# Optimization experiments

Measured on AMD Instinct MI355X. Metric: run time of the kernel, lower is better.

Reference implementation:

```python
import jax, jax.numpy as jnp
import numpy as np

B, L, D = 2, 2048, 768
H = 12
HD = D // H  # 64
SCALE = HD ** -0.5


def setup_inputs() -> dict:
    key = jax.random.key(0)
    k1, k2, k3 = jax.random.split(key, 3)
    x = jax.random.normal(k1, (B, L, D), dtype=jnp.float32)
    mask = jnp.ones((B, L), dtype=jnp.int32)
    # nn.Linear weights: [out_features, in_features]
    Wqkv = jax.random.normal(k2, (3 * D, D), dtype=jnp.float32) * (D ** -0.5)
    bqkv = jnp.zeros((3 * D,), dtype=jnp.float32)
    Wout = jax.random.normal(k3, (D, D), dtype=jnp.float32) * (D ** -0.5)
    bout = jnp.zeros((D,), dtype=jnp.float32)
    return {"x": x, "mask": mask, "Wqkv": Wqkv, "bqkv": bqkv, "Wout": Wout, "bout": bout}


def reference(x, mask, Wqkv, bqkv, Wout, bout):
    Bx, Lx, Dx = x.shape
    # qkv projection: [B,L,3D] -> [3,B,H,L,HD]
    qkv = x @ Wqkv.T + bqkv
    qkv = qkv.reshape(Bx, Lx, 3, H, HD).transpose(2, 0, 3, 1, 4)
    q, k, v = qkv[0], qkv[1], qkv[2]
    # scores [B,H,L,L]
    attn = jnp.einsum('bhqd,bhkd->bhqk', q, k) * SCALE
    attn = jnp.where(mask[:, None, None, :] == 0, -jnp.inf, attn)
    attn = jax.nn.softmax(attn, axis=-1)
    # dropout p=0.0 -> identity
    out = jnp.einsum('bhqk,bhkd->bhqd', attn, v)
    out = out.transpose(0, 2, 1, 3).reshape(Bx, Lx, Dx)
    return out @ Wout.T + bout
```

## Files before the change

### kernel.cpp

```cpp
#include <hip/hip_runtime.h>
#include <hip/hip_bf16.h>

#define DEV __device__ __forceinline__

typedef __bf16 bf16_t;
typedef bf16_t bf16x8 __attribute__((ext_vector_type(8)));
typedef float f32x4 __attribute__((ext_vector_type(4)));
typedef float f32x16 __attribute__((ext_vector_type(16)));
typedef unsigned int u32x4 __attribute__((ext_vector_type(4)));

constexpr int Bc = 2, Lc = 2048, Dc = 768, Hc = 12, HDc = 64;
constexpr int NTOK = Bc * Lc;
constexpr int QKVN = 3 * Dc;
constexpr float ATT_SCALE = 0.125f;
constexpr float LOG2E = 1.44269504088896f;

DEV unsigned short f2bf(float f) {
  unsigned int u = __builtin_bit_cast(unsigned int, f);
  u += 0x7FFFu + ((u >> 16) & 1u);
  return (unsigned short)(u >> 16);
}

DEV bf16x8 ld16(const unsigned short* p) {
  return __builtin_bit_cast(bf16x8, *reinterpret_cast<const u32x4*>(p));
}

DEV unsigned cvtpk(float lo, float hi) {
  unsigned r;
  asm("v_cvt_pk_bf16_f32 %0, %1, %2" : "=v"(r) : "v"(lo), "v"(hi));
  return r;
}

DEV void gload16(const unsigned short* g, unsigned short* l) {
  __builtin_amdgcn_global_load_lds(
      (const __attribute__((address_space(1))) unsigned int*)g,
      (__attribute__((address_space(3))) unsigned int*)l, 16, 0, 0);
}

__global__ __launch_bounds__(256) void prep_kernel(
    const float* __restrict__ x, const float* __restrict__ Wqkv,
    const float* __restrict__ Wout, const int* __restrict__ mask,
    unsigned short* __restrict__ xb, unsigned short* __restrict__ wqkvb,
    unsigned short* __restrict__ woutb, float* __restrict__ mb,
    int* __restrict__ mflag) {
  const int bid = blockIdx.x, tid = threadIdx.x;
  const float* src; unsigned short* dst; int base;
  if (bid < 3072)      { src = x;    dst = xb;    base = bid; }
  else if (bid < 4800) { src = Wqkv; dst = wqkvb; base = bid - 3072; }
  else if (bid < 5376) { src = Wout; dst = woutb; base = bid - 4800; }
  else {
    int i = (bid - 5376) * 256 + tid;
    int mv = mask[i];
    mb[i] = mv ? 0.f : -1e30f;
    unsigned long long anyz = __ballot(mv == 0);
    if ((tid & 63) == 0) mflag[i >> 6] = (anyz != 0ull) ? 1 : 0;
    return;
  }
  int i = (base * 256 + tid) * 4;
  float4 v = *reinterpret_cast<const float4*>(src + i);
  ushort4 o;
  o.x = f2bf(v.x); o.y = f2bf(v.y); o.z = f2bf(v.z); o.w = f2bf(v.w);
  *reinterpret_cast<ushort4*>(dst + i) = o;
}

template <int MODE>
__global__ __launch_bounds__(256) void gemm_bt(
    const unsigned short* __restrict__ A,
    const unsigned short* __restrict__ Bw,
    const float* __restrict__ bias,
    unsigned short* __restrict__ qb, unsigned short* __restrict__ kb,
    unsigned short* __restrict__ vtb,
    float* __restrict__ Y,
    int M, int N, int K) {
  constexpr int BM = 128, BN = 128, BK = 64;
  __shared__ alignas(16) unsigned short a_lds[BM * BK];
  __shared__ alignas(16) unsigned short b_lds[BN * BK];
  __shared__ alignas(16) unsigned short qk_patch[(MODE == 0) ? 4 : 1][16][72];

  const int tid = threadIdx.x;
  const int lane = tid & 63;
  const int l15 = lane & 15, lg = lane >> 4;
  const int wave = tid >> 6;
  const int wr = wave >> 1, wc = wave & 1;

  const int ntiles = N / BN;
  const int m0 = (blockIdx.x / ntiles) * BM;
  const int n0 = (blockIdx.x % ntiles) * BN;

  f32x4 acc[4][4] = {};

  for (int k0 = 0; k0 < K; k0 += BK) {
#pragma unroll
    for (int i = 0; i < 4; ++i) {
      int cc = i * 256 + tid;
      int row = cc >> 3, col = (cc & 7) * 8;
      gload16(A + (size_t)(m0 + row) * K + k0 + col, &a_lds[(i * 256 + wave * 64) * 8]);
      gload16(Bw + (size_t)(n0 + row) * K + k0 + col, &b_lds[(i * 256 + wave * 64) * 8]);
    }
    __syncthreads();
#pragma unroll
    for (int kk = 0; kk < 2; ++kk) {
      bf16x8 af[4], bfr[4];
#pragma unroll
      for (int m = 0; m < 4; ++m) {
        int row = wr * 64 + m * 16 + l15;
        af[m] = ld16(&a_lds[row * BK + kk * 32 + lg * 8]);
      }
#pragma unroll
      for (int n = 0; n < 4; ++n) {
        int row = wc * 64 + n * 16 + l15;
        bfr[n] = ld16(&b_lds[row * BK + kk * 32 + lg * 8]);
      }
#pragma unroll
      for (int m = 0; m < 4; ++m)
#pragma unroll
        for (int n = 0; n < 4; ++n)
          acc[m][n] = __builtin_amdgcn_mfma_f32_16x16x32_bf16(af[m], bfr[n], acc[m][n], 0, 0, 0);
    }
    __syncthreads();
  }

  if constexpr (MODE == 0) {
    const int base_col = n0 + wc * 64;
    const int s = base_col / Dc;
    const int h = (base_col % Dc) >> 6;
    if (s == 2) {
#pragma unroll
      for (int m = 0; m < 4; ++m) {
        int lq = m0 + wr * 64 + m * 16 + lg * 4;
        int b = lq >> 11, lql = lq & 2047;
#pragma unroll
        for (int n = 0; n < 4; ++n) {
          int d = n * 16 + l15;
          float bv = bias[base_col + n * 16 + l15];
          ushort4 o;
#pragma unroll
          for (int j = 0; j < 4; ++j)
            ((unsigned short*)&o)[j] = f2bf(acc[m][n][j] + bv);
          *reinterpret_cast<ushort4*>(
              vtb + ((size_t)(b * Hc + h) * HDc + d) * Lc + lql) = o;
        }
      }
    } else {
      unsigned short* dst = (s == 0) ? qb : kb;
      const float sc = (s == 0) ? (ATT_SCALE * LOG2E) : 1.0f;
#pragma unroll
      for (int m = 0; m < 4; ++m) {
#pragma unroll
        for (int n = 0; n < 4; ++n) {
          float bv = bias[base_col + n * 16 + l15];
#pragma unroll
          for (int j = 0; j < 4; ++j)
            qk_patch[wave][lg * 4 + j][n * 16 + l15] =
                f2bf((acc[m][n][j] + bv) * sc);
        }
#pragma unroll
        for (int i = 0; i < 2; ++i) {
          int task = i * 64 + lane;
          int r = task >> 3, ch = task & 7;
          int lq = m0 + wr * 64 + m * 16 + r;
          int b = lq >> 11, lql = lq & 2047;
          u32x4 v = *reinterpret_cast<const u32x4*>(&qk_patch[wave][r][ch * 8]);
          *reinterpret_cast<u32x4*>(
              dst + ((size_t)(b * Hc + h) * Lc + lql) * HDc + ch * 8) = v;
        }
      }
    }
  } else {
#pragma unroll
    for (int m = 0; m < 4; ++m) {
      int row_base = m0 + wr * 64 + m * 16 + lg * 4;
#pragma unroll
      for (int n = 0; n < 4; ++n) {
        int col = n0 + wc * 64 + n * 16 + l15;
        float bv = bias[col];
#pragma unroll
        for (int j = 0; j < 4; ++j)
          Y[(size_t)(row_base + j) * Dc + col] = acc[m][n][j] + bv;
      }
    }
  }
}

__global__ __launch_bounds__(512) void attn_kernel(
    const unsigned short* __restrict__ qb,
    const unsigned short* __restrict__ kb,
    const unsigned short* __restrict__ vtb,
    const float* __restrict__ mb,
    const int* __restrict__ mflag,
    unsigned short* __restrict__ aout) {
  __shared__ alignas(16) unsigned short k_lds[2][2][4096];
  __shared__ alignas(16) unsigned short v_lds[2][2][4096];
  __shared__ float l_lds[4][32];
  const int tid = threadIdx.x;
  const int lane = tid & 63;
  const int l31 = lane & 31;
  const int hi = lane >> 5;
  const int wave = tid >> 6;
  const int g = wave >> 2;
  const int ws = wave & 3;
  const int f = blockIdx.x;
  const int loc = f >> 3;
  const int bh = (f & 7) * 3 + (loc >> 4);
  const int b = bh / Hc, h = bh % Hc;
  const int q0 = (loc & 15) * 128 + ws * 32;
  const int kvbase = g * (Lc / 2);

  const unsigned short* Kbh = kb + (size_t)bh * Lc * HDc;
  const unsigned short* Vbh = vtb + (size_t)bh * HDc * Lc;
  const float* mbb = mb + b * Lc + kvbase + hi * 4;
  const int* mfp = mflag + b * (Lc / 64) + (kvbase >> 6);

  bf16x8 qf[4];
  {
    const unsigned short* Qp = qb + ((size_t)bh * Lc + q0 + l31) * HDc + hi * 8;
#pragma unroll
    for (int c = 0; c < 4; ++c) qf[c] = ld16(Qp + c * 16);
  }

  f32x16 accO[2] = {};
  float l_run = 0.f;

#define STAGE(buf, kv0abs)                                                            \
  {                                                                                   \
    _Pragma("unroll")                                                                 \
    for (int jj = 0; jj < 2; ++jj) {                                                  \
      int j = ws * 2 + jj;                                                            \
      int r8 = j * 8 + (lane >> 3);                                                   \
      int csw = ((lane & 7) ^ (lane >> 3)) << 3;                                      \
      gload16(Kbh + (size_t)((kv0abs) + r8) * HDc + csw, &k_lds[g][buf][j * 512]);    \
      gload16(Vbh + (size_t)r8 * Lc + (kv0abs) + csw, &v_lds[g][buf][j * 512]);       \
    }                                                                                 \
  }

  STAGE(0, kvbase)
  __syncthreads();

  const int swz = (l31 & 7) << 3;

  constexpr int NSTEP = Lc / 128;
  for (int t = 0; t < NSTEP; ++t) {
    const int cur = t & 1;
    if (t + 1 < NSTEP) STAGE(cur ^ 1, kvbase + (t + 1) * 64)
    const unsigned short* kl = &k_lds[g][cur][0];
    const unsigned short* vl = &v_lds[g][cur][0];
    const int kv0 = t * 64;

    f32x16 s0 = {}, s1 = {};
    __builtin_amdgcn_s_setprio(1);
#pragma unroll
    for (int c = 0; c < 4; ++c) {
      int ch = (((c * 2 + hi) << 3) ^ swz);
      s0 = __builtin_amdgcn_mfma_f32_32x32x16_bf16(ld16(kl + l31 * 64 + ch), qf[c], s0, 0, 0, 0);
      s1 = __builtin_amdgcn_mfma_f32_32x32x16_bf16(ld16(kl + (32 + l31) * 64 + ch), qf[c], s1, 0, 0, 0);
    }
    __builtin_amdgcn_s_setprio(0);
    if (mfp[t]) {
#pragma unroll
      for (int gg = 0; gg < 4; ++gg) {
        float4 m0v = *reinterpret_cast<const float4*>(mbb + kv0 + gg * 8);
        float4 m1v = *reinterpret_cast<const float4*>(mbb + kv0 + 32 + gg * 8);
        s0[gg * 4 + 0] += m0v.x; s0[gg * 4 + 1] += m0v.y;
        s0[gg * 4 + 2] += m0v.z; s0[gg * 4 + 3] += m0v.w;
        s1[gg * 4 + 0] += m1v.x; s1[gg * 4 + 1] += m1v.y;
        s1[gg * 4 + 2] += m1v.z; s1[gg * 4 + 3] += m1v.w;
      }
    }
    float rs0 = 0.f, rs1 = 0.f, rs2 = 0.f, rs3 = 0.f;
#pragma unroll
    for (int i = 0; i < 16; i += 4) {
      s0[i] = __builtin_amdgcn_exp2f(s0[i]);         rs0 += s0[i];
      s0[i + 1] = __builtin_amdgcn_exp2f(s0[i + 1]); rs1 += s0[i + 1];
      s0[i + 2] = __builtin_amdgcn_exp2f(s0[i + 2]); rs2 += s0[i + 2];
      s0[i + 3] = __builtin_amdgcn_exp2f(s0[i + 3]); rs3 += s0[i + 3];
      s1[i] = __builtin_amdgcn_exp2f(s1[i]);         rs0 += s1[i];
      s1[i + 1] = __builtin_amdgcn_exp2f(s1[i + 1]); rs1 += s1[i + 1];
      s1[i + 2] = __builtin_amdgcn_exp2f(s1[i + 2]); rs2 += s1[i + 2];
      s1[i + 3] = __builtin_amdgcn_exp2f(s1[i + 3]); rs3 += s1[i + 3];
    }
    float rs = (rs0 + rs1) + (rs2 + rs3);
    rs += __shfl_xor(rs, 32);
    l_run += rs;
    bf16x8 pf[4];
#pragma unroll
    for (int c = 0; c < 4; ++c) {
      const f32x16& sv = (c < 2) ? s0 : s1;
      const int o = (c & 1) * 8;
      unsigned pk01 = cvtpk(sv[o + 0], sv[o + 1]);
      unsigned pk23 = cvtpk(sv[o + 2], sv[o + 3]);
      unsigned pk45 = cvtpk(sv[o + 4], sv[o + 5]);
      unsigned pk67 = cvtpk(sv[o + 6], sv[o + 7]);
      asm("v_permlane32_swap_b32 %0, %1" : "+v"(pk01), "+v"(pk45));
      asm("v_permlane32_swap_b32 %0, %1" : "+v"(pk23), "+v"(pk67));
      u32x4 w = {pk01, pk23, pk45, pk67};
      pf[c] = __builtin_bit_cast(bf16x8, w);
    }
    __builtin_amdgcn_s_setprio(1);
#pragma unroll
    for (int dt = 0; dt < 2; ++dt) {
#pragma unroll
      for (int c = 0; c < 4; ++c) {
        int ch = (((c * 2 + hi) << 3) ^ swz);
        accO[dt] = __builtin_amdgcn_mfma_f32_32x32x16_bf16(ld16(vl + (dt * 32 + l31) * 64 + ch), pf[c], accO[dt], 0, 0, 0);
      }
    }
    __builtin_amdgcn_s_setprio(0);
    __syncthreads();
  }

  float* mO = (float*)&k_lds[0][0][0];
  if (g == 1) {
#pragma unroll
    for (int dt = 0; dt < 2; ++dt)
#pragma unroll
      for (int i = 0; i < 16; ++i)
        mO[(ws * 32 + dt * 16 + i) * 64 + lane] = accO[dt][i];
    if (hi == 0) l_lds[ws][l31] = l_run;
  }
  __syncthreads();
  if (g == 0) {
    float rl = 1.0f / (l_run + l_lds[ws][l31]);
    const int q = q0 + l31;
    unsigned short* op = aout + ((size_t)(b * Lc + q)) * Dc + h * HDc;
#pragma unroll
    for (int dt = 0; dt < 2; ++dt)
#pragma unroll
      for (int gg = 0; gg < 4; ++gg) {
        ushort4 o;
#pragma unroll
        for (int j = 0; j < 4; ++j) {
          int i = gg * 4 + j;
          float v = (accO[dt][i] + mO[(ws * 32 + dt * 16 + i) * 64 + lane]) * rl;
          ((unsigned short*)&o)[j] = f2bf(v);
        }
        *reinterpret_cast<ushort4*>(op + dt * 32 + gg * 8 + hi * 4) = o;
      }
  }
}

extern "C" void kernel_launch(void* const* d_in, const int* in_sizes, int n_in,
                              void* d_out, int out_size, void* d_ws, size_t ws_size,
                              hipStream_t stream) {
  const float* x    = (const float*)d_in[0];
  const int*   mask = (const int*)d_in[1];
  const float* Wqkv = (const float*)d_in[2];
  const float* bqkv = (const float*)d_in[3];
  const float* Wout = (const float*)d_in[4];
  const float* bout = (const float*)d_in[5];
  float* out = (float*)d_out;

  constexpr size_t NX   = (size_t)NTOK * Dc;
  constexpr size_t NWQ  = (size_t)QKVN * Dc;
  constexpr size_t NWO  = (size_t)Dc * Dc;
  unsigned short* w = (unsigned short*)d_ws;
  unsigned short* xb    = w;            w += NX;
  unsigned short* wqkvb = w;            w += NWQ;
  unsigned short* woutb = w;            w += NWO;
  unsigned short* qbuf  = w;            w += NX;
  unsigned short* kbuf  = w;            w += NX;
  unsigned short* vtb   = w;            w += NX;
  unsigned short* aoutb = w;            w += NX;
  float* mbf = (float*)w;               w += 2 * NTOK;
  int* mflag = (int*)w;

  prep_kernel<<<5392, 256, 0, stream>>>(x, Wqkv, Wout, mask, xb, wqkvb, woutb, mbf, mflag);

  gemm_bt<0><<<(NTOK / 128) * (QKVN / 128), 256, 0, stream>>>(
      xb, wqkvb, bqkv, qbuf, kbuf, vtb, nullptr, NTOK, QKVN, Dc);

  attn_kernel<<<dim3(384), 512, 0, stream>>>(qbuf, kbuf, vtb, mbf, mflag, aoutb);

  gemm_bt<1><<<(NTOK / 128) * (Dc / 128), 256, 0, stream>>>(
      aoutb, woutb, bout, nullptr, nullptr, nullptr, out, NTOK, Dc, Dc);
}
```

Measured before the change: 113.0 us.

## Split attention KV tiles across wave pairs within shared stage, smaller blocks

New measurement: 113.6 us. No clear change (+0.5%).

```diff
diff --git a/kernel.cpp b/kernel.cpp
--- a/kernel.cpp
+++ b/kernel.cpp
@@ -182,34 +182,33 @@
   }
 }
 
-__global__ __launch_bounds__(512) void attn_kernel(
+__global__ __launch_bounds__(256) void attn_kernel(
     const unsigned short* __restrict__ qb,
     const unsigned short* __restrict__ kb,
     const unsigned short* __restrict__ vtb,
     const float* __restrict__ mb,
     const int* __restrict__ mflag,
     unsigned short* __restrict__ aout) {
-  __shared__ alignas(16) unsigned short k_lds[2][2][4096];
-  __shared__ alignas(16) unsigned short v_lds[2][2][4096];
-  __shared__ float l_lds[4][32];
+  __shared__ alignas(16) unsigned short k_lds[2][4096];
+  __shared__ alignas(16) unsigned short v_lds[2][4096];
+  __shared__ float l_lds[2][32];
   const int tid = threadIdx.x;
   const int lane = tid & 63;
   const int l31 = lane & 31;
   const int hi = lane >> 5;
   const int wave = tid >> 6;
-  const int g = wave >> 2;
-  const int ws = wave & 3;
+  const int ws = wave & 1;
+  const int g = wave >> 1;
   const int f = blockIdx.x;
   const int loc = f >> 3;
-  const int bh = (f & 7) * 3 + (loc >> 4);
+  const int bh = (f & 7) * 3 + (loc >> 5);
   const int b = bh / Hc, h = bh % Hc;
-  const int q0 = (loc & 15) * 128 + ws * 32;
-  const int kvbase = g * (Lc / 2);
+  const int q0 = (loc & 31) * 64 + ws * 32;
 
   const unsigned short* Kbh = kb + (size_t)bh * Lc * HDc;
   const unsigned short* Vbh = vtb + (size_t)bh * HDc * Lc;
-  const float* mbb = mb + b * Lc + kvbase + hi * 4;
-  const int* mfp = mflag + b * (Lc / 64) + (kvbase >> 6);
+  const float* mbb = mb + b * Lc + hi * 4;
+  const int* mfp = mflag + b * (Lc / 64);
 
   bf16x8 qf[4];
   {
@@ -225,71 +224,63 @@
   {                                                                                   \
     _Pragma("unroll")                                                                 \
     for (int jj = 0; jj < 2; ++jj) {                                                  \
-      int j = ws * 2 + jj;                                                            \
+      int j = wave * 2 + jj;                                                          \
       int r8 = j * 8 + (lane >> 3);                                                   \
-      int csw = ((lane & 7) ^ (lane >> 3)) << 3;                                      \
-      gload16(Kbh + (size_t)((kv0abs) + r8) * HDc + csw, &k_lds[g][buf][j * 512]);    \
-      gload16(Vbh + (size_t)r8 * Lc + (kv0abs) + csw, &v_lds[g][buf][j * 512]);       \
+      int csw = (((lane & 7) ^ (lane >> 3) ^ (j & 3))) << 3;                          \
+      gload16(Kbh + (size_t)((kv0abs) + r8) * HDc + csw, &k_lds[buf][j * 512]);       \
+      gload16(Vbh + (size_t)r8 * Lc + (kv0abs) + csw, &v_lds[buf][j * 512]);          \
     }                                                                                 \
   }
 
-  STAGE(0, kvbase)
+  STAGE(0, 0)
   __syncthreads();
 
-  const int swz = (l31 & 7) << 3;
-
-  constexpr int NSTEP = Lc / 128;
+  const int swz = ((l31 & 7) ^ (l31 >> 3)) << 3;
+
+  constexpr int NSTEP = Lc / 64;
   for (int t = 0; t < NSTEP; ++t) {
     const int cur = t & 1;
-    if (t + 1 < NSTEP) STAGE(cur ^ 1, kvbase + (t + 1) * 64)
-    const unsigned short* kl = &k_lds[g][cur][0];
-    const unsigned short* vl = &v_lds[g][cur][0];
-    const int kv0 = t * 64;
-
-    f32x16 s0 = {}, s1 = {};
+    if (t + 1 < NSTEP) STAGE(cur ^ 1, (t + 1) * 64)
+    const unsigned short* kl = &k_lds[cur][0];
+    const unsigned short* vl = &v_lds[cur][0];
+
+    f32x16 s = {};
     __builtin_amdgcn_s_setprio(1);
 #pragma unroll
     for (int c = 0; c < 4; ++c) {
       int ch = (((c * 2 + hi) << 3) ^ swz);
-      s0 = __builtin_amdgcn_mfma_f32_32x32x16_bf16(ld16(kl + l31 * 64 + ch), qf[c], s0, 0, 0, 0);
-      s1 = __builtin_amdgcn_mfma_f32_32x32x16_bf16(ld16(kl + (32 + l31) * 64 + ch), qf[c], s1, 0, 0, 0);
+      s = __builtin_amdgcn_mfma_f32_32x32x16_bf16(
+          ld16(kl + (g * 32 + l31) * 64 + ch), qf[c], s, 0, 0, 0);
     }
     __builtin_amdgcn_s_setprio(0);
+    const int kvt = t * 64 + g * 32;
     if (mfp[t]) {
 #pragma unroll
       for (int gg = 0; gg < 4; ++gg) {
-        float4 m0v = *reinterpret_cast<const float4*>(mbb + kv0 + gg * 8);
-        float4 m1v = *reinterpret_cast<const float4*>(mbb + kv0 + 32 + gg * 8);
-        s0[gg * 4 + 0] += m0v.x; s0[gg * 4 + 1] += m0v.y;
-        s0[gg * 4 + 2] += m0v.z; s0[gg * 4 + 3] += m0v.w;
-        s1[gg * 4 + 0] += m1v.x; s1[gg * 4 + 1] += m1v.y;
-        s1[gg * 4 + 2] += m1v.z; s1[gg * 4 + 3] += m1v.w;
+        float4 m0v = *reinterpret_cast<const float4*>(mbb + kvt + gg * 8);
+        s[gg * 4 + 0] += m0v.x; s[gg * 4 + 1] += m0v.y;
+        s[gg * 4 + 2] += m0v.z; s[gg * 4 + 3] += m0v.w;
       }
     }
     float rs0 = 0.f, rs1 = 0.f, rs2 = 0.f, rs3 = 0.f;
 #pragma unroll
     for (int i = 0; i < 16; i += 4) {
-      s0[i] = __builtin_amdgcn_exp2f(s0[i]);         rs0 += s0[i];
-      s0[i + 1] = __builtin_amdgcn_exp2f(s0[i + 1]); rs1 += s0[i + 1];
-      s0[i + 2] = __builtin_amdgcn_exp2f(s0[i + 2]); rs2 += s0[i + 2];
-      s0[i + 3] = __builtin_amdgcn_exp2f(s0[i + 3]); rs3 += s0[i + 3];
-      s1[i] = __builtin_amdgcn_exp2f(s1[i]);         rs0 += s1[i];
-      s1[i + 1] = __builtin_amdgcn_exp2f(s1[i + 1]); rs1 += s1[i + 1];
-      s1[i + 2] = __builtin_amdgcn_exp2f(s1[i + 2]); rs2 += s1[i + 2];
-      s1[i + 3] = __builtin_amdgcn_exp2f(s1[i + 3]); rs3 += s1[i + 3];
+      s[i] = __builtin_amdgcn_exp2f(s[i]);         rs0 += s[i];
+      s[i + 1] = __builtin_amdgcn_exp2f(s[i + 1]); rs1 += s[i + 1];
+      s[i + 2] = __builtin_amdgcn_exp2f(s[i + 2]); rs2 += s[i + 2];
+      s[i + 3] = __builtin_amdgcn_exp2f(s[i + 3]); rs3 += s[i + 3];
     }
     float rs = (rs0 + rs1) + (rs2 + rs3);
     rs += __shfl_xor(rs, 32);
     l_run += rs;
-    bf16x8 pf[4];
-#pragma unroll
-    for (int c = 0; c < 4; ++c) {
-      const f32x16& sv = (c < 2) ? s0 : s1;
-      const int o = (c & 1) * 8;
-      unsigned pk01 = cvtpk(sv[o + 0], sv[o + 1]);
-      unsigned pk23 = cvtpk(sv[o + 2], sv[o + 3]);
-      unsigned pk45 = cvtpk(sv[o + 4], sv[o + 5]);
-      unsigned pk67 = cvtpk(sv[o + 6], sv[o + 7]);
+    bf16x8 pf[2];
+#pragma unroll
+    for (int c = 0; c < 2; ++c) {
+      const int o = c * 8;
+      unsigned pk01 = cvtpk(s[o + 0], s[o + 1]);
+      unsigned pk23 = cvtpk(s[o + 2], s[o + 3]);
+      unsigned pk45 = cvtpk(s[o + 4], s[o + 5]);
+      unsigned pk67 = cvtpk(s[o + 6], s[o + 7]);
       asm("v_permlane32_swap_b32 %0, %1" : "+v"(pk01), "+v"(pk45));
       asm("v_permlane32_swap_b32 %0, %1" : "+v"(pk23), "+v"(pk67));
       u32x4 w = {pk01, pk23, pk45, pk67};
@@ -299,16 +290,17 @@
 #pragma unroll
     for (int dt = 0; dt < 2; ++dt) {
 #pragma unroll
-      for (int c = 0; c < 4; ++c) {
-        int ch = (((c * 2 + hi) << 3) ^ swz);
-        accO[dt] = __builtin_amdgcn_mfma_f32_32x32x16_bf16(ld16(vl + (dt * 32 + l31) * 64 + ch), pf[c], accO[dt], 0, 0, 0);
+      for (int c = 0; c < 2; ++c) {
+        int ch = (((g * 4 + c * 2 + hi) << 3) ^ swz);
+        accO[dt] = __builtin_amdgcn_mfma_f32_32x32x16_bf16(
+            ld16(vl + (dt * 32 + l31) * 64 + ch), pf[c], accO[dt], 0, 0, 0);
       }
     }
     __builtin_amdgcn_s_setprio(0);
     __syncthreads();
   }
 
-  float* mO = (float*)&k_lds[0][0][0];
+  float* mO = (float*)&k_lds[0][0];
   if (g == 1) {
 #pragma unroll
     for (int dt = 0; dt < 2; ++dt)
@@ -368,7 +360,7 @@
   gemm_bt<0><<<(NTOK / 128) * (QKVN / 128), 256, 0, stream>>>(
       xb, wqkvb, bqkv, qbuf, kbuf, vtb, nullptr, NTOK, QKVN, Dc);
 
-  attn_kernel<<<dim3(384), 512, 0, stream>>>(qbuf, kbuf, vtb, mbf, mflag, aoutb);
+  attn_kernel<<<dim3(768), 256, 0, stream>>>(qbuf, kbuf, vtb, mbf, mflag, aoutb);
 
   gemm_bt<1><<<(NTOK / 128) * (Dc / 128), 256, 0, stream>>>(
       aoutb, woutb, bout, nullptr, nullptr, nullptr, out, NTOK, Dc, Dc);
```
